# Performance work log

Hardware: AMD Instinct MI355X
Metric: run time of the kernel (lower is better)

## Reference

```python
import jax, jax.numpy as jnp
import numpy as np

# module config (init_kwargs)
AH, AW = 14, 14            # aligned_height, aligned_width
SCALE = 0.25               # spatial_scale
RATIO = 2                  # sampling_ratio
SHIFT = 0.0                # spatial_shift (added in feature-map coords)
HALF_PART = 0              # 0 = full box
ROI_SCALE = 1.0            # box rescale about its center


def setup_inputs() -> dict:
    key = jax.random.key(0)
    kf, kb, kx, ky, kw, kh = jax.random.split(key, 6)
    B, C, H, W = 2, 256, 200, 272
    N = 256
    features = jax.random.normal(kf, (B, C, H, W), dtype=jnp.float32)
    img_h, img_w = H / SCALE, W / SCALE
    bidx = jax.random.randint(kb, (N,), 0, B).astype(jnp.float32)
    x1 = jax.random.uniform(kx, (N,)) * (img_w * 0.6)
    y1 = jax.random.uniform(ky, (N,)) * (img_h * 0.6)
    bw = 32.0 + jax.random.uniform(kw, (N,)) * (img_w * 0.35)
    bh = 32.0 + jax.random.uniform(kh, (N,)) * (img_h * 0.35)
    rois = jnp.stack([bidx, x1, y1, x1 + bw, y1 + bh], axis=1).astype(jnp.float32)
    return {"features": features, "rois": rois}


def _lin_idx(coord, size):
    # bilinear index/weight prep with RoIAlign boundary rules
    valid = (coord > -1.0) & (coord < float(size))
    c = jnp.clip(coord, 0.0, float(size - 1))
    lo = jnp.floor(c)
    hi = jnp.minimum(lo + 1.0, float(size - 1))
    frac = c - lo
    return lo.astype(jnp.int32), hi.astype(jnp.int32), frac, valid.astype(coord.dtype)


def _roi_mask_align(features, rois):
    B, C, H, W = features.shape
    N = rois.shape[0]
    PH, PW, r = AH + 1, AW + 1, RATIO
    b = rois[:, 0].astype(jnp.int32)
    # to feature-map coords, with roi_scale about the box center and spatial_shift
    x1, y1, x2, y2 = (rois[:, 1] * SCALE, rois[:, 2] * SCALE,
                      rois[:, 3] * SCALE, rois[:, 4] * SCALE)
    cx, cy = 0.5 * (x1 + x2), 0.5 * (y1 + y2)
    hw, hh = 0.5 * (x2 - x1) * ROI_SCALE, 0.5 * (y2 - y1) * ROI_SCALE
    x1, x2 = cx - hw + SHIFT, cx + hw + SHIFT
    y1, y2 = cy - hh + SHIFT, cy + hh + SHIFT
    roi_w = jnp.maximum(x2 - x1, 1.0)
    roi_h = jnp.maximum(y2 - y1, 1.0)
    bin_w = roi_w / PW
    bin_h = roi_h / PH
    # sample coords, separable: sx [N, PW*r], sy [N, PH*r]
    ix = jnp.arange(PW * r, dtype=jnp.float32)
    iy = jnp.arange(PH * r, dtype=jnp.float32)
    sx = x1[:, None] + (ix[None, :] + 0.5) * (bin_w[:, None] / r)
    sy = y1[:, None] + (iy[None, :] + 0.5) * (bin_h[:, None] / r)
    y_lo, y_hi, fy, vy = _lin_idx(sy, H)
    x_lo, x_hi, fx, vx = _lin_idx(sx, W)
    featsT = jnp.transpose(features, (0, 2, 3, 1))  # [B,H,W,C]
    bb = b[:, None, None]
    gather = lambda yi, xi: featsT[bb, yi[:, :, None], xi[:, None, :]]  # [N,Sy,Sx,C]
    wy0, wy1 = 1.0 - fy, fy
    wx0, wx1 = 1.0 - fx, fx
    val = (gather(y_lo, x_lo) * (wy0[:, :, None] * wx0[:, None, :])[..., None]
           + gather(y_lo, x_hi) * (wy0[:, :, None] * wx1[:, None, :])[..., None]
           + gather(y_hi, x_lo) * (wy1[:, :, None] * wx0[:, None, :])[..., None]
           + gather(y_hi, x_hi) * (wy1[:, :, None] * wx1[:, None, :])[..., None])
    val = val * (vy[:, :, None] * vx[:, None, :])[..., None]
    # average the r*r samples per bin -> [N, PH, PW, C]
    val = val.reshape(N, PH, r, PW, r, C).mean(axis=(2, 4))
    return jnp.transpose(val, (0, 3, 1, 2))  # [N, C, PH, PW]


def reference(features, rois):
    x = _roi_mask_align(features, rois)  # [N, C, AH+1, AW+1]
    # avg_pool2d(kernel=2, stride=1)
    out = 0.25 * (x[..., :-1, :-1] + x[..., 1:, :-1]
                  + x[..., :-1, 1:] + x[..., 1:, 1:])
    return out  # [N, C, AH, AW]
```

## Files before the change

kernel.cpp:

```cpp
#include <hip/hip_runtime.h>


#define AH_  14
#define AW_  14
#define C_   256
#define H_   200
#define W_   272
#define HW_  (H_ * W_)
#define CPW  2
#define CPB  4
#define NPAIR 15

__global__ __launch_bounds__(128, 8)
void roi_mask_align_avg_kernel(const float* __restrict__ feat,
                               const float* __restrict__ rois,
                               float* __restrict__ out) {
    __shared__ float Ls[2][CPW * AH_ * AW_];

    const int p   = blockIdx.x;
    const int xcd = p & 7;
    const int q   = p >> 3;
    const int n   = q & 255;
    const int cgi = q >> 8;
    const int cg  = cgi * 8 + xcd;
    const int c0  = cg * CPB;

    const int tid  = threadIdx.x;
    const int wave = tid >> 6;
    const int lane = tid & 63;
    const int half = lane >> 5;
    const int ix   = lane & 31;

    const float r0f = rois[n * 5 + 0];
    const float x1s = rois[n * 5 + 1] * 0.25f;
    const float y1s = rois[n * 5 + 2] * 0.25f;
    const float x2s = rois[n * 5 + 3] * 0.25f;
    const float y2s = rois[n * 5 + 4] * 0.25f;
    const int   b   = (int)r0f;

    const float cx = 0.5f * (x1s + x2s), cy = 0.5f * (y1s + y2s);
    const float hw = 0.5f * (x2s - x1s), hh = 0.5f * (y2s - y1s);
    const float x1 = cx - hw, x2 = cx + hw;
    const float y1 = cy - hh, y2 = cy + hh;
    const float roi_w = fmaxf(x2 - x1, 1.0f);
    const float roi_h = fmaxf(y2 - y1, 1.0f);
    const float sub_w = roi_w * (1.0f / 15.0f) * 0.5f;
    const float sub_h = roi_h * (1.0f / 15.0f) * 0.5f;

    const float sx  = x1 + ((float)ix + 0.5f) * sub_w;
    const bool  vx_ = (sx > -1.0f) && (sx < (float)W_) && (ix < 30);
    const float ccx = fminf(fmaxf(sx, 0.0f), (float)(W_ - 1));
    const float lox = floorf(ccx);
    const int   xl  = (int)lox;
    const int   xh  = min(xl + 1, W_ - 1);
    const float fx  = ccx - lox;
    const float vmx = vx_ ? 1.0f : 0.0f;
    const float wx0 = (1.0f - fx) * vmx;
    const float wx1 = fx * vmx;

    const int cW = c0 + wave * CPW;
    const float* __restrict__ bp = feat + ((size_t)b * C_ + cW) * (size_t)HW_;
    const int vx0 = half * HW_ + xl;
    const int vx1 = half * HW_ + xh;

    const int  aw   = ix >> 1;
    const int  so   = half * (AH_ * AW_) + aw;
    const bool emit = ((lane & 1) == 0) && (aw < AW_);
    float* __restrict__ Lw = Ls[wave];

    float prevS = 0.0f;

    #pragma unroll
    for (int k = 0; k < NPAIR; ++k) {
        float P = 0.0f;
        #pragma unroll
        for (int r = 0; r < 2; ++r) {
            const int iy = 2 * k + r;
            const float sy  = y1 + ((float)iy + 0.5f) * sub_h;
            const bool  vy_ = (sy > -1.0f) && (sy < (float)H_);
            const float ccy = fminf(fmaxf(sy, 0.0f), (float)(H_ - 1));
            const float loy = floorf(ccy);
            const int   yl  = (int)loy;
            const int   yh  = min(yl + 1, H_ - 1);
            const float fy  = ccy - loy;
            const float vmy = vy_ ? 1.0f : 0.0f;
            const float wy0 = (1.0f - fy) * vmy;
            const float wy1 = fy * vmy;

            const int ro0 = __builtin_amdgcn_readfirstlane(yl * W_);
            const int ro1 = __builtin_amdgcn_readfirstlane(yh * W_);
            const float* __restrict__ r0p = bp + ro0;
            const float* __restrict__ r1p = bp + ro1;

            const float w00 = wy0 * wx0, w01 = wy0 * wx1;
            const float w10 = wy1 * wx0, w11 = wy1 * wx1;

            P += r0p[vx0] * w00 + r0p[vx1] * w01
               + r1p[vx0] * w10 + r1p[vx1] * w11;
        }
        const float t = P + __shfl_xor(P, 1, 64);
        const float u = t + __shfl_down(t, 2, 64);
        if (k > 0 && emit) {
            Lw[so + (k - 1) * AW_] = (prevS + u) * 0.0625f;
        }
        prevS = u;
    }

    float* __restrict__ op = out + ((size_t)n * C_ + cW) * (AH_ * AW_);
    for (int o = lane; o < CPW * AH_ * AW_; o += 64) {
        op[o] = Lw[o];
    }
}

extern "C" void kernel_launch(void* const* d_in, const int* in_sizes, int n_in,
                              void* d_out, int out_size, void* d_ws, size_t ws_size,
                              hipStream_t stream) {
    const float* feat = (const float*)d_in[0];
    const float* rois = (const float*)d_in[1];
    float* out = (float*)d_out;
    const int grid = 256 * (C_ / CPB);
    roi_mask_align_avg_kernel<<<grid, 128, 0, stream>>>(feat, rois, out);
}
```

Measured before the change: 267.4 us.

## Split output rows across waves and reuse shared feature rows between samples

The split of work inside a block changes from channels to output rows. Each wave now covers all four channels of the block but only half of the sample rows (16 sample rows for 7 output rows). The kernel also caches the loaded low and high row values in registers and skips or shifts loads when consecutive samples fall on the same or adjacent feature rows, which is meant to cut redundant global loads for small ROIs. The cost is data-dependent branches, a non-unrolled loop, more live registers, and two overlapping sample rows recomputed between the waves.

```diff
diff --git a/kernel.cpp b/kernel.cpp
--- a/kernel.cpp
+++ b/kernel.cpp
@@ -7,15 +7,13 @@
 #define H_   200
 #define W_   272
 #define HW_  (H_ * W_)
-#define CPW  2
 #define CPB  4
-#define NPAIR 15
 
 __global__ __launch_bounds__(128, 8)
 void roi_mask_align_avg_kernel(const float* __restrict__ feat,
                                const float* __restrict__ rois,
                                float* __restrict__ out) {
-    __shared__ float Ls[2][CPW * AH_ * AW_];
+    __shared__ float Ls[2][CPB * 7 * AW_];
 
     const int p   = blockIdx.x;
     const int xcd = p & 7;
@@ -58,57 +56,81 @@
     const float wx0 = (1.0f - fx) * vmx;
     const float wx1 = fx * vmx;
 
-    const int cW = c0 + wave * CPW;
-    const float* __restrict__ bp = feat + ((size_t)b * C_ + cW) * (size_t)HW_;
+    const float* __restrict__ bpA = feat + ((size_t)b * C_ + c0) * (size_t)HW_;
+    const float* __restrict__ bpB = bpA + 2 * HW_;
     const int vx0 = half * HW_ + xl;
     const int vx1 = half * HW_ + xh;
 
     const int  aw   = ix >> 1;
-    const int  so   = half * (AH_ * AW_) + aw;
     const bool emit = ((lane & 1) == 0) && (aw < AW_);
     float* __restrict__ Lw = Ls[wave];
 
-    float prevS = 0.0f;
+    float alo0 = 0.f, alo1 = 0.f, ahi0 = 0.f, ahi1 = 0.f;
+    float blo0 = 0.f, blo1 = 0.f, bhi0 = 0.f, bhi1 = 0.f;
+    int   pyl = -100, pyh = -100;
 
-    #pragma unroll
-    for (int k = 0; k < NPAIR; ++k) {
-        float P = 0.0f;
+    const int iy0 = wave * 14;
+    float prevSA = 0.f, prevSB = 0.f;
+
+    for (int kk = 0; kk < 8; ++kk) {
+        float PA = 0.f, PB = 0.f;
         #pragma unroll
         for (int r = 0; r < 2; ++r) {
-            const int iy = 2 * k + r;
+            const int iy = iy0 + 2 * kk + r;
             const float sy  = y1 + ((float)iy + 0.5f) * sub_h;
             const bool  vy_ = (sy > -1.0f) && (sy < (float)H_);
             const float ccy = fminf(fmaxf(sy, 0.0f), (float)(H_ - 1));
             const float loy = floorf(ccy);
-            const int   yl  = (int)loy;
-            const int   yh  = min(yl + 1, H_ - 1);
             const float fy  = ccy - loy;
             const float vmy = vy_ ? 1.0f : 0.0f;
             const float wy0 = (1.0f - fy) * vmy;
             const float wy1 = fy * vmy;
 
-            const int ro0 = __builtin_amdgcn_readfirstlane(yl * W_);
-            const int ro1 = __builtin_amdgcn_readfirstlane(yh * W_);
-            const float* __restrict__ r0p = bp + ro0;
-            const float* __restrict__ r1p = bp + ro1;
+            const int yl_s = __builtin_amdgcn_readfirstlane((int)loy);
+            const int yh_s = min(yl_s + 1, H_ - 1);
+
+            if (yl_s == pyl && yh_s == pyh) {
+            } else if (yl_s == pyh) {
+                alo0 = ahi0; alo1 = ahi1; blo0 = bhi0; blo1 = bhi1;
+                const float* __restrict__ pa = bpA + yh_s * W_;
+                const float* __restrict__ pb = bpB + yh_s * W_;
+                ahi0 = pa[vx0]; ahi1 = pa[vx1];
+                bhi0 = pb[vx0]; bhi1 = pb[vx1];
+            } else {
+                const float* __restrict__ pal = bpA + yl_s * W_;
+                const float* __restrict__ pah = bpA + yh_s * W_;
+                const float* __restrict__ pbl = bpB + yl_s * W_;
+                const float* __restrict__ pbh = bpB + yh_s * W_;
+                alo0 = pal[vx0]; alo1 = pal[vx1];
+                ahi0 = pah[vx0]; ahi1 = pah[vx1];
+                blo0 = pbl[vx0]; blo1 = pbl[vx1];
+                bhi0 = pbh[vx0]; bhi1 = pbh[vx1];
+            }
+            pyl = yl_s; pyh = yh_s;
 
             const float w00 = wy0 * wx0, w01 = wy0 * wx1;
             const float w10 = wy1 * wx0, w11 = wy1 * wx1;
-
-            P += r0p[vx0] * w00 + r0p[vx1] * w01
-               + r1p[vx0] * w10 + r1p[vx1] * w11;
+            PA += alo0 * w00 + alo1 * w01 + ahi0 * w10 + ahi1 * w11;
+            PB += blo0 * w00 + blo1 * w01 + bhi0 * w10 + bhi1 * w11;
         }
-        const float t = P + __shfl_xor(P, 1, 64);
-        const float u = t + __shfl_down(t, 2, 64);
-        if (k > 0 && emit) {
-            Lw[so + (k - 1) * AW_] = (prevS + u) * 0.0625f;
+        const float tA = PA + __shfl_xor(PA, 1, 64);
+        const float uA = tA + __shfl_down(tA, 2, 64);
+        const float tB = PB + __shfl_xor(PB, 1, 64);
+        const float uB = tB + __shfl_down(tB, 2, 64);
+        if (kk > 0 && emit) {
+            const int row = kk - 1;
+            Lw[half * 98 + row * AW_ + aw]       = (prevSA + uA) * 0.0625f;
+            Lw[(2 + half) * 98 + row * AW_ + aw] = (prevSB + uB) * 0.0625f;
         }
-        prevS = u;
+        prevSA = uA;
+        prevSB = uB;
     }
 
-    float* __restrict__ op = out + ((size_t)n * C_ + cW) * (AH_ * AW_);
-    for (int o = lane; o < CPW * AH_ * AW_; o += 64) {
-        op[o] = Lw[o];
+    float* __restrict__ op = out + ((size_t)n * C_ + c0) * (AH_ * AW_);
+    for (int o = lane; o < CPB * 7 * AW_; o += 64) {
+        const int ch  = o / 98;
+        const int rem = o - ch * 98;
+        op[ch * (AH_ * AW_) + wave * 98 + rem] = Lw[o];
     }
 }
 
```

New measurement: 245.5 us. 8.2% less time.
